# Performance work log

Hardware: AMD Instinct MI355X
Metric: run time of the kernel (lower is better)

The kernel has to match this reference:

```python
import jax, jax.numpy as jnp
import numpy as np

VOCAB = 10000
EMB = 100
UNITS = 64
SEQ = 80
BATCH = 4096


def lstm_scan(x, W, U, b):
    """Keras-style LSTM. x: [B,T,D]; W: [D,4U]; U: [U,4U]; b: [4U].
    Gate order i, f, g(cell), o. Returns full hidden sequence [B,T,U]."""
    B = x.shape[0]
    units = U.shape[0]
    xT = jnp.swapaxes(x, 0, 1)  # [T,B,D]

    def step(carry, xt):
        h, c = carry
        z = xt @ W + h @ U + b  # [B,4U]
        i, f, g, o = jnp.split(z, 4, axis=-1)
        c = jax.nn.sigmoid(f) * c + jax.nn.sigmoid(i) * jnp.tanh(g)
        h = jax.nn.sigmoid(o) * jnp.tanh(c)
        return (h, c), h

    init = (jnp.zeros((B, units), x.dtype), jnp.zeros((B, units), x.dtype))
    _, hs = jax.lax.scan(step, init, xT)
    return jnp.swapaxes(hs, 0, 1)  # [B,T,U]


def setup_inputs() -> dict:
    key = jax.random.key(0)
    ks = jax.random.split(key, 10)
    tokens = jax.random.randint(ks[0], (BATCH, SEQ), 0, VOCAB, dtype=jnp.int32)
    s = 0.05
    emb = jax.random.normal(ks[1], (VOCAB, EMB), jnp.float32) * s
    W1 = jax.random.normal(ks[2], (EMB, 4 * UNITS), jnp.float32) * s
    U1 = jax.random.normal(ks[3], (UNITS, 4 * UNITS), jnp.float32) * s
    b1 = jnp.zeros((4 * UNITS,), jnp.float32)
    W2 = jax.random.normal(ks[4], (UNITS, 4 * UNITS), jnp.float32) * s
    U2 = jax.random.normal(ks[5], (UNITS, 4 * UNITS), jnp.float32) * s
    b2 = jnp.zeros((4 * UNITS,), jnp.float32)
    Wd = jax.random.normal(ks[6], (UNITS, 1), jnp.float32) * s
    bd = jnp.zeros((1,), jnp.float32)
    return {"tokens": tokens, "emb": emb, "W1": W1, "U1": U1, "b1": b1,
            "W2": W2, "U2": U2, "b2": b2, "Wd": Wd, "bd": bd}


def reference(tokens, emb, W1, U1, b1, W2, U2, b2, Wd, bd):
    x = emb[tokens]                      # [B,T,EMB]
    h1 = lstm_scan(x, W1, U1, b1)        # [B,T,U] (dropout inactive at inference)
    h2 = lstm_scan(h1, W2, U2, b2)       # [B,T,U]
    hlast = h2[:, -1, :]                 # second LSTM has return_sequences=False
    logits = hlast @ Wd + bd             # [B,1]
    return jax.nn.sigmoid(logits)
```

## Files before the change

kernel.cpp:

```cpp
#include <hip/hip_runtime.h>


#define VOCAB 10000
#define EMB   100
#define SEQ   80
#define BATCH 4096
#define NGRID 512

typedef _Float16 f16;
typedef _Float16 f16x8 __attribute__((ext_vector_type(8)));
typedef _Float16 half2_t __attribute__((ext_vector_type(2)));
typedef float    f32x4 __attribute__((ext_vector_type(4)));
typedef unsigned int uint;

#define LOG2E 1.4426950408889634f

__device__ __forceinline__ uint pack2(float lo, float hi) {
    return __builtin_bit_cast(uint, __builtin_amdgcn_cvt_pkrtz(lo, hi));
}
__device__ __forceinline__ uint rl_u(uint v, int l) { return (uint)__builtin_amdgcn_readlane((int)v, l); }
__device__ __forceinline__ float dot2(uint a, uint b, float c) {
    return __builtin_amdgcn_fdot2(__builtin_bit_cast(half2_t, a), __builtin_bit_cast(half2_t, b), c, false);
}
__device__ __forceinline__ f32x4 mfma16(uint4 a, uint4 b, f32x4 c) {
    return __builtin_amdgcn_mfma_f32_16x16x32_f16(
        __builtin_bit_cast(f16x8, a), __builtin_bit_cast(f16x8, b), c, 0, 0, 0);
}
__device__ __forceinline__ void barrier_lds() {
    asm volatile("s_waitcnt lgkmcnt(0)\n\ts_barrier" ::: "memory");
}
__device__ __forceinline__ float sigm_e(float x) {
    float t = __builtin_amdgcn_exp2f(-LOG2E * x);
    return __builtin_amdgcn_rcpf(1.0f + t);
}
__device__ __forceinline__ float tanh_e(float x) {
    float t = __builtin_amdgcn_exp2f((2.0f * LOG2E) * x);
    return __builtin_fmaf(-2.0f, __builtin_amdgcn_rcpf(1.0f + t), 1.0f);
}
__device__ __forceinline__ float sigm_exact(float x) {
    return 1.0f / (1.0f + __expf(-x));
}

#define WS_E1F_OFF 0
#define WS_B1F_OFF 10240000
#define WS_B2F_OFF 10272768
#define WS_NEEDED  10338304

#define NB_E1 512
__global__ __launch_bounds__(256) void prep_e1(
    const float* __restrict__ emb,
    const float* __restrict__ W1, const float* __restrict__ U1,
    const float* __restrict__ b1,
    const float* __restrict__ W2, const float* __restrict__ U2,
    float* __restrict__ E1f, uint* __restrict__ B1f, uint* __restrict__ B2f) {
    if (blockIdx.x < NB_E1) {
        const int c    = threadIdx.x;
        const int lane = c & 63;
        uint w[50];
#pragma unroll
        for (int kp = 0; kp < 50; ++kp)
            w[kp] = pack2(W1[(2 * kp) * 256 + c], W1[(2 * kp + 1) * 256 + c]);
        const float bias = b1[c];
        const int   dst  = (c & 63) * 4 + (c >> 6);
        float2 ecur = {0.f, 0.f};
        if (lane < 50) ecur = *(const float2*)(emb + (size_t)blockIdx.x * EMB + 2 * lane);
        for (int v = blockIdx.x; v < VOCAB; v += NB_E1) {
            float2 enext = {0.f, 0.f};
            if (v + NB_E1 < VOCAB && lane < 50)
                enext = *(const float2*)(emb + (size_t)(v + NB_E1) * EMB + 2 * lane);
            uint ep = pack2(ecur.x, ecur.y);
            float a0 = bias, a1 = 0.0f;
#pragma unroll
            for (int kp = 0; kp < 50; kp += 2) {
                a0 = dot2(w[kp],     rl_u(ep, kp),     a0);
                a1 = dot2(w[kp + 1], rl_u(ep, kp + 1), a1);
            }
            E1f[v * 256 + dst] = a0 + a1;
            ecur = enext;
        }
    } else {
        int idx = (blockIdx.x - NB_E1) * 256 + threadIdx.x;
        if (idx < 8192) {
            int dw = idx & 3, lane = (idx >> 2) & 63, kt = (idx >> 8) & 1,
                g = (idx >> 9) & 3, w = idx >> 11;
            int k   = kt * 32 + (lane >> 4) * 8 + dw * 2;
            int col = g * 64 + w * 16 + (lane & 15);
            B1f[idx] = pack2(U1[k * 256 + col], U1[(k + 1) * 256 + col]);
        }
        if (idx < 16384) {
            int dw = idx & 3, lane = (idx >> 2) & 63, kt = (idx >> 8) & 3,
                g = (idx >> 10) & 3, w = idx >> 12;
            int k   = kt * 32 + (lane >> 4) * 8 + dw * 2;
            int col = g * 64 + w * 16 + (lane & 15);
            float lo = (k < 64) ? W2[k * 256 + col] : U2[(k - 64) * 256 + col];
            float hi = (k < 63) ? W2[(k + 1) * 256 + col] : U2[(k + 1 - 64) * 256 + col];
            B2f[idx] = pack2(lo, hi);
        }
    }
}

__global__ __launch_bounds__(256, 2) void lstm_mfma(
    const int* __restrict__ tokens, const f32x4* __restrict__ E1f4,
    const uint4* __restrict__ B1f, const uint4* __restrict__ B2f,
    const float* __restrict__ b2, const float* __restrict__ Wd,
    const float* __restrict__ bd, float* __restrict__ out) {
    __shared__ uint4 AbufU[512];
    __shared__ float red[32];
    f16* Abuf = (f16*)AbufU;

    const int tid  = threadIdx.x;
    const int w    = tid >> 6;
    const int lane = tid & 63;
    const int q    = lane >> 4;
    const int li   = lane & 15;
    const int u    = w * 16 + li;
    const int row0 = blockIdx.x * 8;

    const uint4 z4 = {0u, 0u, 0u, 0u};
    AbufU[tid] = z4; AbufU[tid + 256] = z4;

    uint4 b1f[4][2], b2f[4][4];
#pragma unroll
    for (int g = 0; g < 4; ++g) {
#pragma unroll
        for (int kt = 0; kt < 2; ++kt) b1f[g][kt] = B1f[((w * 4 + g) * 2 + kt) * 64 + lane];
#pragma unroll
        for (int kt = 0; kt < 4; ++kt) b2f[g][kt] = B2f[((w * 4 + g) * 4 + kt) * 64 + lane];
    }
    float b2v[4];
#pragma unroll
    for (int g = 0; g < 4; ++g) b2v[g] = b2[g * 64 + u];
    const float wdv = Wd[u];
    const float bdv = bd[0];

    int4  tokc[2], tokn[2];
    f32x4 e1buf[2][2];
#pragma unroll
    for (int r = 0; r < 2; ++r) {
        tokc[r] = *(const int4*)(tokens + (size_t)(row0 + q * 2 + r) * SEQ);
        e1buf[0][r] = E1f4[(size_t)tokc[r].x * 64 + u];
        e1buf[1][r] = E1f4[(size_t)tokc[r].y * 64 + u];
    }

    float c1[2] = {0.f, 0.f}, c2[2] = {0.f, 0.f};
    float h2v[2] = {0.f, 0.f};
    uint4 a1f0 = z4, a1f1 = z4, a2f0 = z4, a2f1 = z4;

    __syncthreads();

#pragma unroll 1
    for (int t4 = 0; t4 < SEQ / 4; ++t4) {
        if (t4 < SEQ / 4 - 1) {
#pragma unroll
            for (int r = 0; r < 2; ++r)
                tokn[r] = *(const int4*)(tokens + (size_t)(row0 + q * 2 + r) * SEQ + (t4 + 1) * 4);
        }
#pragma unroll
        for (int s = 0; s < 4; ++s) {
            const int p = s & 1;
            f32x4 acc[4];
#pragma unroll
            for (int g = 0; g < 4; ++g) {
                acc[g][0] = e1buf[p][0][g];
                acc[g][1] = e1buf[p][1][g];
            }
#pragma unroll
            for (int g = 0; g < 4; ++g) acc[g] = mfma16(a1f0, b1f[g][0], acc[g]);
#pragma unroll
            for (int g = 0; g < 4; ++g) acc[g] = mfma16(a1f1, b1f[g][1], acc[g]);

            f32x4 acc2[4];
#pragma unroll
            for (int g = 0; g < 4; ++g) {
                acc2[g][0] = b2v[g];
                acc2[g][1] = b2v[g];
            }
#pragma unroll
            for (int g = 0; g < 4; ++g) acc2[g] = mfma16(a1f0, b2f[g][0], acc2[g]);
#pragma unroll
            for (int g = 0; g < 4; ++g) acc2[g] = mfma16(a1f1, b2f[g][1], acc2[g]);
#pragma unroll
            for (int g = 0; g < 4; ++g) acc2[g] = mfma16(a2f0, b2f[g][2], acc2[g]);
#pragma unroll
            for (int g = 0; g < 4; ++g) acc2[g] = mfma16(a2f1, b2f[g][3], acc2[g]);

#pragma unroll
            for (int r = 0; r < 2; ++r) {
                float ig = sigm_e(acc[0][r]);
                float fg = sigm_e(acc[1][r]);
                float gv = tanh_e(acc[2][r]);
                float og = sigm_e(acc[3][r]);
                c1[r] = fg * c1[r] + ig * gv;
                float h1 = og * tanh_e(c1[r]);
                Abuf[p * 2048 + ((u >> 3) * 16 + 4 * q + r) * 8 + (u & 7)] = (f16)h1;
            }

            if (t4 | s) {
#pragma unroll
                for (int r = 0; r < 2; ++r) {
                    float ig = sigm_e(acc2[0][r]);
                    float fg = sigm_e(acc2[1][r]);
                    float gv = tanh_e(acc2[2][r]);
                    float og = sigm_e(acc2[3][r]);
                    c2[r] = fg * c2[r] + ig * gv;
                    h2v[r] = og * tanh_e(c2[r]);
                    Abuf[p * 2048 + 1024 + ((u >> 3) * 16 + 4 * q + r) * 8 + (u & 7)] = (f16)h2v[r];
                }
            }

            if (t4 * 4 + s + 2 < SEQ) {
#pragma unroll
                for (int r = 0; r < 2; ++r) {
                    int tk = (s == 0) ? tokc[r].z : (s == 1) ? tokc[r].w
                           : (s == 2) ? tokn[r].x : tokn[r].y;
                    e1buf[p][r] = E1f4[(size_t)tk * 64 + u];
                }
            }

            barrier_lds();

            a1f0 = AbufU[p * 256 + lane];
            a1f1 = AbufU[p * 256 + 64 + lane];
            a2f0 = AbufU[p * 256 + 128 + lane];
            a2f1 = AbufU[p * 256 + 192 + lane];
        }
#pragma unroll
        for (int r = 0; r < 2; ++r) tokc[r] = tokn[r];
    }

    {
        f32x4 acc2[4];
#pragma unroll
        for (int g = 0; g < 4; ++g) {
            acc2[g][0] = b2v[g];
            acc2[g][1] = b2v[g];
        }
#pragma unroll
        for (int g = 0; g < 4; ++g) acc2[g] = mfma16(a1f0, b2f[g][0], acc2[g]);
#pragma unroll
        for (int g = 0; g < 4; ++g) acc2[g] = mfma16(a1f1, b2f[g][1], acc2[g]);
#pragma unroll
        for (int g = 0; g < 4; ++g) acc2[g] = mfma16(a2f0, b2f[g][2], acc2[g]);
#pragma unroll
        for (int g = 0; g < 4; ++g) acc2[g] = mfma16(a2f1, b2f[g][3], acc2[g]);
#pragma unroll
        for (int r = 0; r < 2; ++r) {
            float ig = sigm_e(acc2[0][r]);
            float fg = sigm_e(acc2[1][r]);
            float gv = tanh_e(acc2[2][r]);
            float og = sigm_e(acc2[3][r]);
            c2[r] = fg * c2[r] + ig * gv;
            h2v[r] = og * tanh_e(c2[r]);
        }
    }

#pragma unroll
    for (int r = 0; r < 2; ++r) {
        float pv = h2v[r] * wdv;
        pv += __shfl_xor(pv, 1, 64);
        pv += __shfl_xor(pv, 2, 64);
        pv += __shfl_xor(pv, 4, 64);
        pv += __shfl_xor(pv, 8, 64);
        if (li == 0) red[w * 8 + q * 2 + r] = pv;
    }
    __syncthreads();
    if (tid < 8) {
        float sum = red[tid] + red[8 + tid] + red[16 + tid] + red[24 + tid] + bdv;
        out[row0 + tid] = sigm_exact(sum);
    }
}

__device__ __forceinline__ float lane_bcast(float v, int j) {
    return __builtin_bit_cast(float, __builtin_amdgcn_readlane(__builtin_bit_cast(int, v), j));
}
__device__ __forceinline__ float sigm_f(float x)  { return 1.0f / (1.0f + __expf(-x)); }
__device__ __forceinline__ float tanh_f(float x)  { return 2.0f / (1.0f + __expf(-2.0f * x)) - 1.0f; }

__global__ __launch_bounds__(512) void lstm_fused_fallback(
    const int* __restrict__ tokens, const float* __restrict__ emb,
    const float* __restrict__ W1, const float* __restrict__ U1, const float* __restrict__ b1,
    const float* __restrict__ W2, const float* __restrict__ U2, const float* __restrict__ b2,
    const float* __restrict__ Wd, const float* __restrict__ bd, float* __restrict__ out) {
    const int lane = threadIdx.x & 63;
    const int wave = threadIdx.x >> 6;
    const int row0 = blockIdx.x * 16 + wave * 2;
    float bias1[4], bias2[4];
#pragma unroll
    for (int g = 0; g < 4; ++g) { bias1[g] = b1[g * 64 + lane]; bias2[g] = b2[g * 64 + lane]; }
    const float wd = Wd[lane]; const float bdv = bd[0];
    float h1[2] = {0.f, 0.f}, c1[2] = {0.f, 0.f}, h2[2] = {0.f, 0.f}, c2[2] = {0.f, 0.f};
#pragma unroll 1
    for (int t = 0; t < SEQ; ++t) {
        float acc[4][2];
#pragma unroll
        for (int g = 0; g < 4; ++g) { acc[g][0] = bias1[g]; acc[g][1] = bias1[g]; }
        int tokA = __builtin_amdgcn_readfirstlane(tokens[(row0 + 0) * SEQ + t]);
        int tokB = __builtin_amdgcn_readfirstlane(tokens[(row0 + 1) * SEQ + t]);
        const float4* xA = (const float4*)(emb + (size_t)tokA * EMB);
        const float4* xB = (const float4*)(emb + (size_t)tokB * EMB);
#pragma unroll 5
        for (int d4 = 0; d4 < EMB / 4; ++d4) {
            float4 a4 = xA[d4]; float4 b4 = xB[d4];
            float av[4] = {a4.x, a4.y, a4.z, a4.w}; float bv[4] = {b4.x, b4.y, b4.z, b4.w};
#pragma unroll
            for (int e = 0; e < 4; ++e) {
                const float* wrow = W1 + (d4 * 4 + e) * 256;
#pragma unroll
                for (int g = 0; g < 4; ++g) {
                    float wv = wrow[g * 64 + lane];
                    acc[g][0] += av[e] * wv; acc[g][1] += bv[e] * wv;
                }
            }
        }
#pragma unroll 4
        for (int j = 0; j < 64; ++j) {
            float ha = lane_bcast(h1[0], j), hb = lane_bcast(h1[1], j);
            const float* urow = U1 + j * 256;
#pragma unroll
            for (int g = 0; g < 4; ++g) {
                float wv = urow[g * 64 + lane];
                acc[g][0] += ha * wv; acc[g][1] += hb * wv;
            }
        }
#pragma unroll
        for (int r = 0; r < 2; ++r) {
            float ig = sigm_f(acc[0][r]), fg = sigm_f(acc[1][r]);
            float gg = tanh_f(acc[2][r]), og = sigm_f(acc[3][r]);
            c1[r] = fg * c1[r] + ig * gg; h1[r] = og * tanh_f(c1[r]);
        }
        float acc2[4][2];
#pragma unroll
        for (int g = 0; g < 4; ++g) { acc2[g][0] = bias2[g]; acc2[g][1] = bias2[g]; }
#pragma unroll 4
        for (int j = 0; j < 64; ++j) {
            float pa = lane_bcast(h1[0], j), pb = lane_bcast(h1[1], j);
            float qa = lane_bcast(h2[0], j), qb = lane_bcast(h2[1], j);
            const float* w2row = W2 + j * 256; const float* u2row = U2 + j * 256;
#pragma unroll
            for (int g = 0; g < 4; ++g) {
                float w2v = w2row[g * 64 + lane], u2v = u2row[g * 64 + lane];
                acc2[g][0] += pa * w2v + qa * u2v;
                acc2[g][1] += pb * w2v + qb * u2v;
            }
        }
#pragma unroll
        for (int r = 0; r < 2; ++r) {
            float ig = sigm_f(acc2[0][r]), fg = sigm_f(acc2[1][r]);
            float gg = tanh_f(acc2[2][r]), og = sigm_f(acc2[3][r]);
            c2[r] = fg * c2[r] + ig * gg; h2[r] = og * tanh_f(c2[r]);
        }
    }
#pragma unroll
    for (int r = 0; r < 2; ++r) {
        float p = h2[r] * wd;
#pragma unroll
        for (int off = 32; off > 0; off >>= 1) p += __shfl_down(p, off, 64);
        if (lane == 0) out[row0 + r] = sigm_f(p + bdv);
    }
}

extern "C" void kernel_launch(void* const* d_in, const int* in_sizes, int n_in,
                              void* d_out, int out_size, void* d_ws, size_t ws_size,
                              hipStream_t stream) {
    const int*   tokens = (const int*)  d_in[0];
    const float* emb    = (const float*)d_in[1];
    const float* W1     = (const float*)d_in[2];
    const float* U1     = (const float*)d_in[3];
    const float* b1     = (const float*)d_in[4];
    const float* W2     = (const float*)d_in[5];
    const float* U2     = (const float*)d_in[6];
    const float* b2     = (const float*)d_in[7];
    const float* Wd     = (const float*)d_in[8];
    const float* bd     = (const float*)d_in[9];
    float* out = (float*)d_out;

    if (ws_size < (size_t)WS_NEEDED) {
        lstm_fused_fallback<<<256, 512, 0, stream>>>(tokens, emb, W1, U1, b1, W2, U2, b2, Wd, bd, out);
        return;
    }

    char*  ws  = (char*)d_ws;
    float* E1f = (float*)(ws + WS_E1F_OFF);
    uint*  B1f = (uint*) (ws + WS_B1F_OFF);
    uint*  B2f = (uint*) (ws + WS_B2F_OFF);

    prep_e1  <<<NB_E1 + 64, 256, 0, stream>>>(emb, W1, U1, b1, W2, U2, E1f, B1f, B2f);
    lstm_mfma<<<NGRID, 256, 0, stream>>>(tokens, (const f32x4*)E1f,
                                         (const uint4*)B1f, (const uint4*)B2f,
                                         b2, Wd, bd, out);
}
```

Baseline: 173.7 us.

## Compute embedding-projection table with MFMA tiles instead of per-lane dot2

```diff
diff --git a/kernel.cpp b/kernel.cpp
--- a/kernel.cpp
+++ b/kernel.cpp
@@ -46,40 +46,98 @@
 #define WS_B2F_OFF 10272768
 #define WS_NEEDED  10338304
 
-#define NB_E1 512
+#define NB_GEMM 160
 __global__ __launch_bounds__(256) void prep_e1(
     const float* __restrict__ emb,
     const float* __restrict__ W1, const float* __restrict__ U1,
     const float* __restrict__ b1,
     const float* __restrict__ W2, const float* __restrict__ U2,
     float* __restrict__ E1f, uint* __restrict__ B1f, uint* __restrict__ B2f) {
-    if (blockIdx.x < NB_E1) {
-        const int c    = threadIdx.x;
-        const int lane = c & 63;
-        uint w[50];
-#pragma unroll
-        for (int kp = 0; kp < 50; ++kp)
-            w[kp] = pack2(W1[(2 * kp) * 256 + c], W1[(2 * kp + 1) * 256 + c]);
-        const float bias = b1[c];
-        const int   dst  = (c & 63) * 4 + (c >> 6);
-        float2 ecur = {0.f, 0.f};
-        if (lane < 50) ecur = *(const float2*)(emb + (size_t)blockIdx.x * EMB + 2 * lane);
-        for (int v = blockIdx.x; v < VOCAB; v += NB_E1) {
-            float2 enext = {0.f, 0.f};
-            if (v + NB_E1 < VOCAB && lane < 50)
-                enext = *(const float2*)(emb + (size_t)(v + NB_E1) * EMB + 2 * lane);
-            uint ep = pack2(ecur.x, ecur.y);
-            float a0 = bias, a1 = 0.0f;
-#pragma unroll
-            for (int kp = 0; kp < 50; kp += 2) {
-                a0 = dot2(w[kp],     rl_u(ep, kp),     a0);
-                a1 = dot2(w[kp + 1], rl_u(ep, kp + 1), a1);
-            }
-            E1f[v * 256 + dst] = a0 + a1;
-            ecur = enext;
+    if (blockIdx.x < NB_GEMM) {
+        const int tid  = threadIdx.x;
+        const int w    = tid >> 6;
+        const int lane = tid & 63;
+        const int q    = lane >> 4;
+        const int li   = lane & 15;
+        const int v0b  = blockIdx.x * 64;
+        if (v0b >= VOCAB) return;
+
+        uint4 bf[4][4];
+#pragma unroll
+        for (int nf = 0; nf < 4; ++nf) {
+            const int col = w * 64 + nf * 16 + li;
+#pragma unroll
+            for (int kt = 0; kt < 4; ++kt) {
+                const int k0 = kt * 32 + q * 8;
+                uint dwv[4];
+#pragma unroll
+                for (int dw = 0; dw < 4; ++dw) {
+                    const int k = k0 + 2 * dw;
+                    float lo = (k     < EMB) ? W1[k * 256 + col]       : 0.0f;
+                    float hi = (k + 1 < EMB) ? W1[(k + 1) * 256 + col] : 0.0f;
+                    dwv[dw] = pack2(lo, hi);
+                }
+                bf[nf][kt].x = dwv[0]; bf[nf][kt].y = dwv[1];
+                bf[nf][kt].z = dwv[2]; bf[nf][kt].w = dwv[3];
+            }
+        }
+        float b1v[4];
+#pragma unroll
+        for (int nf = 0; nf < 4; ++nf) b1v[nf] = b1[w * 64 + nf * 16 + li];
+
+#pragma unroll 1
+        for (int mt = 0; mt < 4; ++mt) {
+            const int v0 = v0b + mt * 16;
+            if (v0 >= VOCAB) break;
+            const int vr = v0 + li;
+            const float* er = emb + (size_t)((vr < VOCAB) ? vr : (VOCAB - 1)) * EMB;
+
+            uint4 af[4];
+#pragma unroll
+            for (int kt = 0; kt < 3; ++kt) {
+                const int k0 = kt * 32 + q * 8;
+                float4 lo4 = *(const float4*)(er + k0);
+                float4 hi4 = *(const float4*)(er + k0 + 4);
+                af[kt].x = pack2(lo4.x, lo4.y);
+                af[kt].y = pack2(lo4.z, lo4.w);
+                af[kt].z = pack2(hi4.x, hi4.y);
+                af[kt].w = pack2(hi4.z, hi4.w);
+            }
+            if (q == 0) {
+                float4 t = *(const float4*)(er + 96);
+                af[3].x = pack2(t.x, t.y);
+                af[3].y = pack2(t.z, t.w);
+                af[3].z = 0u; af[3].w = 0u;
+            } else {
+                af[3].x = 0u; af[3].y = 0u; af[3].z = 0u; af[3].w = 0u;
+            }
+
+            f32x4 acc[4];
+#pragma unroll
+            for (int nf = 0; nf < 4; ++nf) {
+                acc[nf][0] = b1v[nf]; acc[nf][1] = b1v[nf];
+                acc[nf][2] = b1v[nf]; acc[nf][3] = b1v[nf];
+            }
+#pragma unroll
+            for (int kt = 0; kt < 4; ++kt)
+#pragma unroll
+                for (int nf = 0; nf < 4; ++nf)
+                    acc[nf] = mfma16(af[kt], bf[nf][kt], acc[nf]);
+
+            const bool full = (v0 + 16 <= VOCAB);
+#pragma unroll
+            for (int nf = 0; nf < 4; ++nf) {
+                const int dst = (nf * 16 + li) * 4 + w;
+#pragma unroll
+                for (int reg = 0; reg < 4; ++reg) {
+                    const int r = v0 + q * 4 + reg;
+                    if (full || r < VOCAB)
+                        E1f[(size_t)r * 256 + dst] = acc[nf][reg];
+                }
+            }
         }
     } else {
-        int idx = (blockIdx.x - NB_E1) * 256 + threadIdx.x;
+        int idx = (blockIdx.x - NB_GEMM) * 256 + threadIdx.x;
         if (idx < 8192) {
             int dw = idx & 3, lane = (idx >> 2) & 63, kt = (idx >> 8) & 1,
                 g = (idx >> 9) & 3, w = idx >> 11;
@@ -384,7 +442,7 @@
     uint*  B1f = (uint*) (ws + WS_B1F_OFF);
     uint*  B2f = (uint*) (ws + WS_B2F_OFF);
 
-    prep_e1  <<<NB_E1 + 64, 256, 0, stream>>>(emb, W1, U1, b1, W2, U2, E1f, B1f, B2f);
+    prep_e1  <<<NB_GEMM + 64, 256, 0, stream>>>(emb, W1, U1, b1, W2, U2, E1f, B1f, B2f);
     lstm_mfma<<<NGRID, 256, 0, stream>>>(tokens, (const f32x4*)E1f,
                                          (const uint4*)B1f, (const uint4*)B2f,
                                          b2, Wd, bd, out);
```

After: 165.7 us. 1.05x faster.
